# Kernel optimization log

Hardware: AMD Instinct MI355X
Metric: run time of the kernel (lower is better)

Reference implementation:

```python
import jax, jax.numpy as jnp
import numpy as np

N = 4096
D_FEAT = 64


def setup_inputs() -> dict:
    key = jax.random.key(0)
    kx, ky = jax.random.split(key)
    xINP = jax.random.normal(kx, (N, D_FEAT), dtype=jnp.float32)
    yINP = jax.random.normal(ky, (N, D_FEAT), dtype=jnp.float32)
    return {"xINP": xINP, "yINP": yINP}


def _greedy_match(xINP, yINP):
    n = xINP.shape[0]
    # Euclidean (p=2) distance matrix, same as scipy.spatial.distance_matrix
    x2 = jnp.sum(xINP * xINP, axis=1)[:, None]           # [n, 1]
    y2 = jnp.sum(yINP * yINP, axis=1)[None, :]           # [1, n]
    sq = jnp.maximum(x2 + y2 - 2.0 * (xINP @ yINP.T), 0.0)
    cost = jnp.sqrt(sq)                                   # [n, n]
    # sorted() with key is stable; jnp.argsort is stable by default
    order = jnp.argsort(cost.reshape(-1))                 # [n*n]

    row0 = jnp.full((n,), -1, dtype=jnp.int32)
    col0 = jnp.full((n,), -1, dtype=jnp.int32)

    def body(k, state):
        row, col = state
        idx = order[k]
        i = idx // n
        j = idx % n
        free = (row[i] == -1) & (col[j] == -1)
        row = row.at[i].set(jnp.where(free, j.astype(jnp.int32), row[i]))
        col = col.at[j].set(jnp.where(free, i.astype(jnp.int32), col[j]))
        return (row, col)

    row, _col = jax.lax.fori_loop(0, n * n, body, (row0, col0))
    return row  # row_to_col_match_vec, int32 in [-1, n)


def reference(xINP, yINP):
    return _greedy_match(xINP, yINP)
```

## Files before the change

### kernel.cpp

```cpp
#include <hip/hip_runtime.h>

#define N 4096
#define D 64
#define TCAP 1024
#define TTHRESH 96
#define SNB 256
#define SNT 512
#define S0B 1024
#define S0T 512
#define RPAIRS 14

typedef unsigned long long u64;

__device__ float g_C[(size_t)N * (size_t)N];
__device__ float g_tailC[(size_t)TCAP * TCAP];
__device__ float4 g_yT[N * 16];
__device__ float g_x2[N], g_y2[N];
__device__ int   g_rowMatch[N];
__device__ int   g_freeRows[2][N];
__device__ int   g_freeCols[2][N];
__device__ int   g_rowBestJ[N];
__device__ u64   g_rowMin0[N];
__device__ u64   g_colMin[2][N];
__device__ int   g_nr[2], g_nc[2];
__device__ int   g_done, g_finalCur;

__device__ inline u64 shfl_down_u64(u64 v, int d) {
  unsigned lo = (unsigned)(v & 0xffffffffull);
  unsigned hi = (unsigned)(v >> 32);
  lo = __shfl_down(lo, d, 64);
  hi = __shfl_down(hi, d, 64);
  return ((u64)hi << 32) | (u64)lo;
}

__device__ inline void block_rowmin_reduce8(u64* best, int rows, u64* s_part) {
  const int tid = threadIdx.x;
  const int lane = tid & 63;
  const int wv = tid >> 6;
#pragma unroll
  for (int r = 0; r < 16; ++r) {
    if (r < rows) {
      u64 v = best[r];
#pragma unroll
      for (int d = 32; d > 0; d >>= 1) {
        u64 o = shfl_down_u64(v, d);
        v = (o < v) ? o : v;
      }
      if (lane == 0) s_part[r * 8 + wv] = v;
    }
  }
  __syncthreads();
  if (tid < rows) {
    u64 mn = s_part[tid * 8];
#pragma unroll
    for (int w = 1; w < 8; ++w) {
      u64 o = s_part[tid * 8 + w];
      mn = (o < mn) ? o : mn;
    }
    s_part[128 + tid] = mn;
  }
}

__device__ __forceinline__ float f4e(const float4* a, int e) {
  float4 v = a[e >> 2];
  switch (e & 3) {
    case 0: return v.x;
    case 1: return v.y;
    case 2: return v.z;
    default: return v.w;
  }
}

__global__ void __launch_bounds__(256) k_init(const float* __restrict__ x,
                                              const float* __restrict__ y) {
  const int i = blockIdx.x * 256 + threadIdx.x;
  const float4* xr4 = reinterpret_cast<const float4*>(x + (size_t)i * D);
  const float4* yr4 = reinterpret_cast<const float4*>(y + (size_t)i * D);

  {
    float4 xv[16];
#pragma unroll
    for (int k = 0; k < 16; ++k) xv[k] = xr4[k];
    float qx[8];
#pragma unroll
    for (int j = 0; j < 8; ++j) {
      float v = f4e(xv, j);
      qx[j] = __fmul_rn(v, v);
    }
#pragma unroll
    for (int m = 8; m < D; m += 8) {
#pragma unroll
      for (int j = 0; j < 8; ++j) {
        float v = f4e(xv, m + j);
        qx[j] = __fadd_rn(qx[j], __fmul_rn(v, v));
      }
    }
    g_x2[i] = __fadd_rn(__fadd_rn(__fadd_rn(qx[0], qx[1]), __fadd_rn(qx[2], qx[3])),
                        __fadd_rn(__fadd_rn(qx[4], qx[5]), __fadd_rn(qx[6], qx[7])));
  }
  {
    float4 yv[16];
#pragma unroll
    for (int k = 0; k < 16; ++k) yv[k] = yr4[k];
    float qy[8];
#pragma unroll
    for (int j = 0; j < 8; ++j) {
      float w = f4e(yv, j);
      qy[j] = __fmul_rn(w, w);
    }
#pragma unroll
    for (int m = 8; m < D; m += 8) {
#pragma unroll
      for (int j = 0; j < 8; ++j) {
        float w = f4e(yv, m + j);
        qy[j] = __fadd_rn(qy[j], __fmul_rn(w, w));
      }
    }
    g_y2[i] = __fadd_rn(__fadd_rn(__fadd_rn(qy[0], qy[1]), __fadd_rn(qy[2], qy[3])),
                        __fadd_rn(__fadd_rn(qy[4], qy[5]), __fadd_rn(qy[6], qy[7])));
#pragma unroll
    for (int k = 0; k < 16; ++k) g_yT[(k << 12) + i] = yv[k];
  }

  g_rowMatch[i] = -1;
  g_freeRows[0][i] = i;
  g_freeCols[0][i] = i;
  g_rowMin0[i] = ~0ull;
  g_colMin[0][i] = ~0ull;
  g_colMin[1][i] = ~0ull;
  if (i == 0) {
    g_nr[0] = N; g_nc[0] = N; g_nr[1] = 0; g_nc[1] = 0;
    g_done = 0;
    g_finalCur = ((RPAIRS & 1) ^ 1);
  }
}

__global__ void __launch_bounds__(S0T) k_scan0(const float* __restrict__ x,
                                               const float* __restrict__ y) {
  __shared__ u64 s_part[64 + 8];
  const int tid = threadIdx.x;
  const int r0 = (blockIdx.x >> 1) << 3;
  const int h = blockIdx.x & 1;

  float x2r[8];
#pragma unroll
  for (int r = 0; r < 8; ++r) x2r[r] = g_x2[r0 + r];
  u64 best[8];
#pragma unroll
  for (int r = 0; r < 8; ++r) best[r] = ~0ull;

  const int c0 = tid + (h << 11);
  float acc[8][4];
#pragma unroll
  for (int r = 0; r < 8; ++r)
#pragma unroll
    for (int k = 0; k < 4; ++k) acc[r][k] = 0.0f;

#pragma unroll
  for (int kc = 0; kc < 16; ++kc) {
    const float4* ytk = g_yT + (kc << 12);
    float4 yv0 = ytk[c0];
    float4 yv1 = ytk[c0 + 512];
    float4 yv2 = ytk[c0 + 1024];
    float4 yv3 = ytk[c0 + 1536];
#pragma unroll
    for (int r = 0; r < 8; ++r) {
      float4 xv = reinterpret_cast<const float4*>(x + (size_t)(r0 + r) * D)[kc];
      acc[r][0] = fmaf(xv.x, yv0.x, acc[r][0]);
      acc[r][0] = fmaf(xv.y, yv0.y, acc[r][0]);
      acc[r][0] = fmaf(xv.z, yv0.z, acc[r][0]);
      acc[r][0] = fmaf(xv.w, yv0.w, acc[r][0]);
      acc[r][1] = fmaf(xv.x, yv1.x, acc[r][1]);
      acc[r][1] = fmaf(xv.y, yv1.y, acc[r][1]);
      acc[r][1] = fmaf(xv.z, yv1.z, acc[r][1]);
      acc[r][1] = fmaf(xv.w, yv1.w, acc[r][1]);
      acc[r][2] = fmaf(xv.x, yv2.x, acc[r][2]);
      acc[r][2] = fmaf(xv.y, yv2.y, acc[r][2]);
      acc[r][2] = fmaf(xv.z, yv2.z, acc[r][2]);
      acc[r][2] = fmaf(xv.w, yv2.w, acc[r][2]);
      acc[r][3] = fmaf(xv.x, yv3.x, acc[r][3]);
      acc[r][3] = fmaf(xv.y, yv3.y, acc[r][3]);
      acc[r][3] = fmaf(xv.z, yv3.z, acc[r][3]);
      acc[r][3] = fmaf(xv.w, yv3.w, acc[r][3]);
    }
  }

#pragma unroll
  for (int k = 0; k < 4; ++k) {
    const int c = c0 + (k << 9);
    const float y2j = g_y2[c];
    u64 ckey = ~0ull;
#pragma unroll
    for (int r = 0; r < 8; ++r) {
      float t = __fadd_rn(x2r[r], y2j);
      float sq = __fsub_rn(t, __fmul_rn(2.0f, acc[r][k]));
      sq = fmaxf(sq, 0.0f);
      float cost = __fsqrt_rn(sq);
      g_C[(size_t)(r0 + r) * N + c] = cost;
      u64 cb = ((u64)__float_as_uint(cost)) << 32;
      u64 rk = cb | (unsigned)c;
      best[r] = (rk < best[r]) ? rk : best[r];
      u64 ck = cb | (unsigned)(r0 + r);
      ckey = (ck < ckey) ? ck : ckey;
    }
    u64 curv = g_colMin[0][c];
    if (ckey < curv) atomicMin((unsigned long long*)&g_colMin[0][c], ckey);
  }

  {
    const int lane = tid & 63, wv = tid >> 6;
#pragma unroll
    for (int r = 0; r < 8; ++r) {
      u64 v = best[r];
#pragma unroll
      for (int d = 32; d > 0; d >>= 1) {
        u64 o = shfl_down_u64(v, d);
        v = (o < v) ? o : v;
      }
      if (lane == 0) s_part[r * 8 + wv] = v;
    }
    __syncthreads();
    if (tid < 8) {
      u64 mn = s_part[tid * 8];
#pragma unroll
      for (int w = 1; w < 8; ++w) {
        u64 o = s_part[tid * 8 + w];
        mn = (o < mn) ? o : mn;
      }
      u64 curv = g_rowMin0[r0 + tid];
      if (mn < curv) atomicMin((unsigned long long*)&g_rowMin0[r0 + tid], mn);
    }
  }
  (void)y;
}

__global__ void __launch_bounds__(SNT, 2) k_scanN(int round) {
  if (g_done) return;
  const int cur = round & 1;
  const int nr = g_nr[cur], nc = g_nc[cur];
  const int tid = threadIdx.x, bid = blockIdx.x;

  for (int t = bid * SNT + tid; t < N; t += SNB * SNT)
    g_colMin[cur ^ 1][t] = ~0ull;

  const int ngroups = (nr + 15) >> 4;
  if (bid >= ngroups) return;
  __shared__ u64 s_colPart[4096];
  __shared__ u64 s_part[128 + 16];
  __shared__ int s_irow[16];

  const int r0 = bid << 4;
  const int rows = min(16, nr - r0);
  if (tid < 16) {
    int rr = (tid < rows) ? (r0 + tid) : r0;
    s_irow[tid] = g_freeRows[cur][rr];
  }
  for (int c = tid; c < nc; c += SNT) s_colPart[c] = ~0ull;
  __syncthreads();

  int ir[16];
#pragma unroll
  for (int r = 0; r < 16; ++r) ir[r] = s_irow[r];
  u64 best[16];
#pragma unroll
  for (int r = 0; r < 16; ++r) best[r] = ~0ull;

  for (int c = tid; c < nc; c += SNT) {
    const int j = g_freeCols[cur][c];
    u64 cpart = s_colPart[c];
#pragma unroll
    for (int r = 0; r < 16; ++r) {
      if (r < rows) {
        float cost = g_C[(size_t)ir[r] * N + j];
        u64 cb = ((u64)__float_as_uint(cost)) << 32;
        u64 rk = cb | (unsigned)j;
        best[r] = (rk < best[r]) ? rk : best[r];
        u64 ck = cb | (unsigned)ir[r];
        cpart = (ck < cpart) ? ck : cpart;
      }
    }
    s_colPart[c] = cpart;
  }

  block_rowmin_reduce8(best, rows, s_part);
  if (tid < rows) g_rowBestJ[s_irow[tid]] = (int)(s_part[128 + tid] & 0xffffffffull);

  for (int c = tid; c < nc; c += SNT) {
    u64 k = s_colPart[c];
    if (k != ~0ull) {
      int j = g_freeCols[cur][c];
      u64 curv = g_colMin[cur][j];
      if (k < curv) atomicMin((unsigned long long*)&g_colMin[cur][j], k);
    }
  }
}

__global__ void __launch_bounds__(SNT) k_match(int round) {
  if (g_done) return;
  const int cur = round & 1, nxt = cur ^ 1;
  const int tid = threadIdx.x, bid = blockIdx.x;
  const int nr = g_nr[cur], nc = g_nc[cur];
  __shared__ int s_wc[8];
  __shared__ int s_base;

  const int lane = tid & 63, wv = tid >> 6;
  if (bid == 0) {
    if (tid == 0) s_base = 0;
    __syncthreads();
    for (int start = 0; start < nr; start += SNT) {
      int r = start + tid;
      int keep = 0; int iv = -1;
      if (r < nr) {
        int i = g_freeRows[cur][r];
        iv = i;
        int j = (round == 0) ? (int)(unsigned)(g_rowMin0[i] & 0xffffffffull)
                             : g_rowBestJ[i];
        u64 cm = g_colMin[cur][j];
        if ((int)(unsigned)(cm & 0xffffffffull) == i) g_rowMatch[i] = j;
        else keep = 1;
      }
      u64 bm = __ballot(keep);
      int pre = __popcll(bm & ((1ull << lane) - 1ull));
      if (lane == 0) s_wc[wv] = __popcll(bm);
      __syncthreads();
      int off = 0, tot = 0;
#pragma unroll
      for (int w = 0; w < 8; ++w) { off += (w < wv) ? s_wc[w] : 0; tot += s_wc[w]; }
      if (keep) g_freeRows[nxt][s_base + off + pre] = iv;
      __syncthreads();
      if (tid == 0) s_base += tot;
      __syncthreads();
    }
    if (tid == 0) {
      int nnr = s_base;
      g_nr[nxt] = nnr;
      if (nnr <= TTHRESH || nnr >= nr) { g_finalCur = nxt; g_done = 1; }
    }
  } else {
    if (tid == 0) s_base = 0;
    __syncthreads();
    for (int start = 0; start < nc; start += SNT) {
      int c = start + tid;
      int keep = 0; int jv = -1;
      if (c < nc) {
        int j = g_freeCols[cur][c];
        jv = j;
        u64 cm = g_colMin[cur][j];
        int i2 = (int)(unsigned)(cm & 0xffffffffull);
        int bj = (round == 0) ? (int)(unsigned)(g_rowMin0[i2] & 0xffffffffull)
                              : g_rowBestJ[i2];
        if (bj != j) keep = 1;
      }
      u64 bm = __ballot(keep);
      int pre = __popcll(bm & ((1ull << lane) - 1ull));
      if (lane == 0) s_wc[wv] = __popcll(bm);
      __syncthreads();
      int off = 0, tot = 0;
#pragma unroll
      for (int w = 0; w < 8; ++w) { off += (w < wv) ? s_wc[w] : 0; tot += s_wc[w]; }
      if (keep) g_freeCols[nxt][s_base + off + pre] = jv;
      __syncthreads();
      if (tid == 0) s_base += tot;
      __syncthreads();
    }
    if (tid == 0) g_nc[nxt] = s_base;
  }
}

__global__ void __launch_bounds__(SNT) k_gather() {
  const int fc = g_finalCur;
  const int mr = g_nr[fc], mc = g_nc[fc];
  if (mr <= 0 || mr > TCAP || mc <= 0 || mc > TCAP) return;
  const int tid = threadIdx.x, bid = blockIdx.x;
  for (int rr = bid; rr < mr; rr += SNB) {
    const int irow = g_freeRows[fc][rr];
    const float* src = g_C + (size_t)irow * N;
    float* dst = g_tailC + (size_t)rr * TCAP;
    for (int c = tid; c < mc; c += SNT) {
      dst[c] = src[g_freeCols[fc][c]];
    }
  }
}

__global__ void __launch_bounds__(1024, 1) k_tail(int* __restrict__ out) {
  __shared__ int s_rpos[2][TCAP], s_cpos[2][TCAP];
  __shared__ int s_rbest[TCAP];
  __shared__ u64 s_cmin[TCAP];
  __shared__ int s_wc[16];
  const int tid = threadIdx.x;
  const int lane = tid & 63, wv = tid >> 6;

  const int fc = g_finalCur;
  int mr = g_nr[fc], mc = g_nc[fc];
  if (mr < 0 || mr > TCAP || mc < 0 || mc > TCAP) mr = 0;
  for (int t = tid; t < mr; t += 1024) s_rpos[0][t] = t;
  for (int t = tid; t < mc; t += 1024) s_cpos[0][t] = t;
  __syncthreads();

  int tcur = 0;
  for (int round = 0; round < 2048 && mr > 0; ++round) {
    const int nit = (mc + 63) >> 6;
    int cpv[16];
#pragma unroll
    for (int k = 0; k < 16; ++k) {
      int ci = (k << 6) + lane;
      cpv[k] = (k < nit && ci < mc) ? s_cpos[tcur][ci] : 0;
    }
    for (int rr = wv; rr < mr; rr += 16) {
      const int rp = s_rpos[tcur][rr];
      const float* rowp = g_tailC + (size_t)rp * TCAP;
      u64 best = ~0ull;
#pragma unroll
      for (int k = 0; k < 16; ++k) {
        if (k < nit) {
          int ci = (k << 6) + lane;
          if (ci < mc) {
            float cost = rowp[cpv[k]];
            u64 key = (((u64)__float_as_uint(cost)) << 32) | (unsigned)ci;
            best = (key < best) ? key : best;
          }
        }
      }
#pragma unroll
      for (int d = 32; d > 0; d >>= 1) {
        u64 o = shfl_down_u64(best, d);
        best = (o < best) ? o : best;
      }
      if (lane == 0) s_rbest[rr] = (int)(best & 0xffffffffull);
    }
    __syncthreads();
    if (tid < mc) {
      const int cp = s_cpos[tcur][tid];
      const float* colp = g_tailC + cp;
      u64 best = ~0ull;
      int r = 0;
      for (; r + 4 <= mr; r += 4) {
#pragma unroll
        for (int q = 0; q < 4; ++q) {
          int rp = s_rpos[tcur][r + q];
          float cost = colp[(size_t)rp * TCAP];
          u64 key = (((u64)__float_as_uint(cost)) << 32) | (unsigned)(r + q);
          best = (key < best) ? key : best;
        }
      }
      for (; r < mr; ++r) {
        int rp = s_rpos[tcur][r];
        float cost = colp[(size_t)rp * TCAP];
        u64 key = (((u64)__float_as_uint(cost)) << 32) | (unsigned)r;
        best = (key < best) ? key : best;
      }
      s_cmin[tid] = best;
    }
    __syncthreads();
    int keep = 0;
    if (tid < mr) {
      int q = s_rbest[tid];
      if ((int)(unsigned)(s_cmin[q] & 0xffffffffull) == tid) {
        g_rowMatch[g_freeRows[fc][s_rpos[tcur][tid]]] = g_freeCols[fc][s_cpos[tcur][q]];
      } else keep = 1;
    }
    u64 bm = __ballot(keep);
    int pre = __popcll(bm & ((1ull << lane) - 1ull));
    if (lane == 0) s_wc[wv] = __popcll(bm);
    __syncthreads();
    int off = 0, tot = 0;
#pragma unroll
    for (int w = 0; w < 16; ++w) { off += (w < wv) ? s_wc[w] : 0; tot += s_wc[w]; }
    if (keep) s_rpos[tcur ^ 1][off + pre] = s_rpos[tcur][tid];
    int newmr = tot;
    __syncthreads();
    int keepc = 0;
    if (tid < mc) {
      int r2 = (int)(unsigned)(s_cmin[tid] & 0xffffffffull);
      if (s_rbest[r2] != tid) keepc = 1;
    }
    u64 bm2 = __ballot(keepc);
    int pre2 = __popcll(bm2 & ((1ull << lane) - 1ull));
    if (lane == 0) s_wc[wv] = __popcll(bm2);
    __syncthreads();
    int off2 = 0, tot2 = 0;
#pragma unroll
    for (int w = 0; w < 16; ++w) { off2 += (w < wv) ? s_wc[w] : 0; tot2 += s_wc[w]; }
    if (keepc) s_cpos[tcur ^ 1][off2 + pre2] = s_cpos[tcur][tid];
    __syncthreads();
    if (newmr >= mr) break;
    mr = newmr; mc = tot2; tcur ^= 1;
  }
  __syncthreads();
  for (int i = tid; i < N; i += 1024) out[i] = g_rowMatch[i];
}

extern "C" void kernel_launch(void* const* d_in, const int* in_sizes, int n_in,
                              void* d_out, int out_size, void* d_ws, size_t ws_size,
                              hipStream_t stream) {
  const float* x = (const float*)d_in[0];
  const float* y = (const float*)d_in[1];
  int* out = (int*)d_out;
  k_init<<<16, 256, 0, stream>>>(x, y);
  k_scan0<<<S0B, S0T, 0, stream>>>(x, y);
  k_match<<<2, SNT, 0, stream>>>(0);
  for (int r = 1; r <= RPAIRS; ++r) {
    k_scanN<<<SNB, SNT, 0, stream>>>(r);
    k_match<<<2, SNT, 0, stream>>>(r);
  }
  k_gather<<<SNB, SNT, 0, stream>>>();
  k_tail<<<1, 1024, 0, stream>>>(out);
  (void)in_sizes; (void)n_in; (void)out_size; (void)d_ws; (void)ws_size;
}
```

Measured before the change: 791.4 us.

## Split free-column scan across multiple blocks per row group in later rounds

When few free rows remain, k_scanN now assigns up to 16 blocks per 16-row group, each handling a strided slice of the free columns, so more of the grid stays busy. Per-row minima can no longer be written directly by one block, so they become double-buffered u64 keys merged with atomicMin, reset each round like the column minima. This adds atomics and an extra buffer clear but aims to cut the serial column loop per block in late rounds.

Measured after the change: 787.7 us. About the same (-0.5%).

```diff
diff --git a/kernel.cpp b/kernel.cpp
--- a/kernel.cpp
+++ b/kernel.cpp
@@ -19,8 +19,7 @@
 __device__ int   g_rowMatch[N];
 __device__ int   g_freeRows[2][N];
 __device__ int   g_freeCols[2][N];
-__device__ int   g_rowBestJ[N];
-__device__ u64   g_rowMin0[N];
+__device__ u64   g_rowMinR[2][N];
 __device__ u64   g_colMin[2][N];
 __device__ int   g_nr[2], g_nc[2];
 __device__ int   g_done, g_finalCur;
@@ -125,7 +124,8 @@
   g_rowMatch[i] = -1;
   g_freeRows[0][i] = i;
   g_freeCols[0][i] = i;
-  g_rowMin0[i] = ~0ull;
+  g_rowMinR[0][i] = ~0ull;
+  g_rowMinR[1][i] = ~0ull;
   g_colMin[0][i] = ~0ull;
   g_colMin[1][i] = ~0ull;
   if (i == 0) {
@@ -227,8 +227,8 @@
         u64 o = s_part[tid * 8 + w];
         mn = (o < mn) ? o : mn;
       }
-      u64 curv = g_rowMin0[r0 + tid];
-      if (mn < curv) atomicMin((unsigned long long*)&g_rowMin0[r0 + tid], mn);
+      u64 curv = g_rowMinR[0][r0 + tid];
+      if (mn < curv) atomicMin((unsigned long long*)&g_rowMinR[0][r0 + tid], mn);
     }
   }
   (void)y;
@@ -240,22 +240,32 @@
   const int nr = g_nr[cur], nc = g_nc[cur];
   const int tid = threadIdx.x, bid = blockIdx.x;
 
-  for (int t = bid * SNT + tid; t < N; t += SNB * SNT)
+  for (int t = bid * SNT + tid; t < N; t += SNB * SNT) {
     g_colMin[cur ^ 1][t] = ~0ull;
+    g_rowMinR[cur ^ 1][t] = ~0ull;
+  }
 
   const int ngroups = (nr + 15) >> 4;
-  if (bid >= ngroups) return;
+  int lgS = 0;
+  while (lgS < 4 && (ngroups << (lgS + 1)) <= SNB) ++lgS;
+  const int S = 1 << lgS;
+  if (bid >= (ngroups << lgS)) return;
+  const int g = bid >> lgS;
+  const int s = bid & (S - 1);
+
   __shared__ u64 s_colPart[4096];
   __shared__ u64 s_part[128 + 16];
   __shared__ int s_irow[16];
 
-  const int r0 = bid << 4;
+  const int r0 = g << 4;
   const int rows = min(16, nr - r0);
   if (tid < 16) {
     int rr = (tid < rows) ? (r0 + tid) : r0;
     s_irow[tid] = g_freeRows[cur][rr];
   }
-  for (int c = tid; c < nc; c += SNT) s_colPart[c] = ~0ull;
+  const int cstart = (s << 9) + tid;
+  const int cstep = S << 9;
+  for (int c = cstart; c < nc; c += cstep) s_colPart[c] = ~0ull;
   __syncthreads();
 
   int ir[16];
@@ -265,7 +275,7 @@
 #pragma unroll
   for (int r = 0; r < 16; ++r) best[r] = ~0ull;
 
-  for (int c = tid; c < nc; c += SNT) {
+  for (int c = cstart; c < nc; c += cstep) {
     const int j = g_freeCols[cur][c];
     u64 cpart = s_colPart[c];
 #pragma unroll
@@ -283,9 +293,13 @@
   }
 
   block_rowmin_reduce8(best, rows, s_part);
-  if (tid < rows) g_rowBestJ[s_irow[tid]] = (int)(s_part[128 + tid] & 0xffffffffull);
-
-  for (int c = tid; c < nc; c += SNT) {
+  if (tid < rows) {
+    u64 k = s_part[128 + tid];
+    u64 curv = g_rowMinR[cur][s_irow[tid]];
+    if (k < curv) atomicMin((unsigned long long*)&g_rowMinR[cur][s_irow[tid]], k);
+  }
+
+  for (int c = cstart; c < nc; c += cstep) {
     u64 k = s_colPart[c];
     if (k != ~0ull) {
       int j = g_freeCols[cur][c];
@@ -313,8 +327,7 @@
       if (r < nr) {
         int i = g_freeRows[cur][r];
         iv = i;
-        int j = (round == 0) ? (int)(unsigned)(g_rowMin0[i] & 0xffffffffull)
-                             : g_rowBestJ[i];
+        int j = (int)(unsigned)(g_rowMinR[cur][i] & 0xffffffffull);
         u64 cm = g_colMin[cur][j];
         if ((int)(unsigned)(cm & 0xffffffffull) == i) g_rowMatch[i] = j;
         else keep = 1;
@@ -347,8 +360,7 @@
         jv = j;
         u64 cm = g_colMin[cur][j];
         int i2 = (int)(unsigned)(cm & 0xffffffffull);
-        int bj = (round == 0) ? (int)(unsigned)(g_rowMin0[i2] & 0xffffffffull)
-                              : g_rowBestJ[i2];
+        int bj = (int)(unsigned)(g_rowMinR[cur][i2] & 0xffffffffull);
         if (bj != j) keep = 1;
       }
       u64 bm = __ballot(keep);
```
